# Kernel optimization log

Measured on AMD Instinct MI355X. Metric: run time of the kernel, lower is better.

Reference implementation:

```python
import jax, jax.numpy as jnp
import numpy as np

B, N, C, H, L, WSZ = 4, 16384, 1024, 16, 256, 512
Dh = C // H
Nb = N // B
NW = Nb // WSZ
EPS = 1e-6
SCALE = Dh ** -0.5


def _ln(h, g=None, b=None):
    m = h.mean(-1, keepdims=True)
    v = h.var(-1, keepdims=True)
    h = (h - m) * jax.lax.rsqrt(v + EPS)
    if g is not None:
        h = h * g + b
    return h


def setup_inputs() -> dict:
    key = jax.random.key(0)
    ks = jax.random.split(key, 16)
    s = 0.02
    return {
        'x': jax.random.normal(ks[0], (N, C), jnp.float32),
        'context': jax.random.normal(ks[1], (B, L, C), jnp.float32),
        'mod': jax.random.normal(ks[2], (B, C), jnp.float32),
        'W_mod': jax.random.normal(ks[3], (C, 6 * C), jnp.float32) * s,
        'b_mod': jnp.zeros((6 * C,), jnp.float32),
        'gamma2': jnp.ones((C,), jnp.float32),
        'beta2': jnp.zeros((C,), jnp.float32),
        'W_qkv': jax.random.normal(ks[4], (C, 3 * C), jnp.float32) * s,
        'b_qkv': jnp.zeros((3 * C,), jnp.float32),
        'W_so': jax.random.normal(ks[5], (C, C), jnp.float32) * s,
        'b_so': jnp.zeros((C,), jnp.float32),
        'W_q': jax.random.normal(ks[6], (C, C), jnp.float32) * s,
        'b_q': jnp.zeros((C,), jnp.float32),
        'W_kv': jax.random.normal(ks[7], (C, 2 * C), jnp.float32) * s,
        'b_kv': jnp.zeros((2 * C,), jnp.float32),
        'W_co': jax.random.normal(ks[8], (C, C), jnp.float32) * s,
        'b_co': jnp.zeros((C,), jnp.float32),
        'W_m1': jax.random.normal(ks[9], (C, 4 * C), jnp.float32) * s,
        'b_m1': jnp.zeros((4 * C,), jnp.float32),
        'W_m2': jax.random.normal(ks[10], (4 * C, C), jnp.float32) * s,
        'b_m2': jnp.zeros((C,), jnp.float32),
    }


def reference(x, context, mod, W_mod, b_mod, gamma2, beta2, W_qkv, b_qkv,
              W_so, b_so, W_q, b_q, W_kv, b_kv, W_co, b_co,
              W_m1, b_m1, W_m2, b_m2):
    xb = x.reshape(B, Nb, C)

    # AdaLN modulation: SiLU -> Linear -> 6 chunks, broadcast per batch item
    m6 = jax.nn.silu(mod) @ W_mod + b_mod                   # [B, 6C]
    sh_msa, sc_msa, g_msa, sh_mlp, sc_mlp, g_mlp = jnp.split(m6, 6, axis=-1)

    # --- windowed sparse self-attention ---
    h = _ln(xb) * (1.0 + sc_msa[:, None]) + sh_msa[:, None]
    qkv = (h @ W_qkv + b_qkv).reshape(B, NW, WSZ, 3, H, Dh)
    q, k, v = qkv[:, :, :, 0], qkv[:, :, :, 1], qkv[:, :, :, 2]
    a = jax.nn.softmax(jnp.einsum('bwqhd,bwkhd->bwhqk', q, k) * SCALE, axis=-1)
    o = jnp.einsum('bwhqk,bwkhd->bwqhd', a, v).reshape(B, Nb, C)
    xb = xb + g_msa[:, None] * (o @ W_so + b_so)

    # --- full cross-attention to per-batch context ---
    h = _ln(xb, gamma2, beta2)
    q = (h @ W_q + b_q).reshape(B, Nb, H, Dh)
    kv = (context @ W_kv + b_kv).reshape(B, L, 2, H, Dh)
    k, v = kv[:, :, 0], kv[:, :, 1]
    a = jax.nn.softmax(jnp.einsum('bqhd,bkhd->bhqk', q, k) * SCALE, axis=-1)
    o = jnp.einsum('bhqk,bkhd->bqhd', a, v).reshape(B, Nb, C)
    xb = xb + (o @ W_co + b_co)

    # --- modulated sparse FFN ---
    h = _ln(xb) * (1.0 + sc_mlp[:, None]) + sh_mlp[:, None]
    h = jax.nn.gelu(h @ W_m1 + b_m1, approximate=True)
    xb = xb + g_mlp[:, None] * (h @ W_m2 + b_m2)

    return xb.reshape(N, C)
```

## Files before the change

### kernel.cpp

```cpp
#include <hip/hip_runtime.h>

typedef unsigned short u16;
typedef __attribute__((ext_vector_type(8))) short short8;
typedef __attribute__((ext_vector_type(4))) float f32x4;

#define SCALE_ 0.125f

struct __align__(8) U16x4 { u16 x, y, z, w; };

__device__ __forceinline__ u16 f2b(float f) {
  union { float f; unsigned u; } c; c.f = f;
  unsigned u = c.u;
  u += 0x7fffu + ((u >> 16) & 1u);
  return (u16)(u >> 16);
}

__device__ __forceinline__ void gload16(const void* g, void* l) {
  __builtin_amdgcn_global_load_lds((const __attribute__((address_space(1))) void*)g,
                                   (__attribute__((address_space(3))) void*)l,
                                   16, 0, 0);
}

__device__ __forceinline__ float gelu_t(float x) {
  float z = 1.5957691216057308f * (x + 0.044715f * x * x * x);
  return x / (1.0f + __expf(-z));
}

__global__ __launch_bounds__(256) void wcast(const float* __restrict__ W,
                                             u16* __restrict__ Wt, int K, int N) {
  __shared__ float t[32][33];
  const int nb = N >> 5;
  const int k0 = (blockIdx.x / nb) << 5;
  const int n0 = (blockIdx.x % nb) << 5;
  const int tx = threadIdx.x & 31;
  const int ty = threadIdx.x >> 5;
#pragma unroll
  for (int r = 0; r < 32; r += 8) t[ty + r][tx] = W[(size_t)(k0 + ty + r) * N + n0 + tx];
  __syncthreads();
#pragma unroll
  for (int r = 0; r < 32; r += 8) Wt[(size_t)(n0 + ty + r) * K + k0 + tx] = f2b(t[tx][ty + r]);
}

__global__ __launch_bounds__(256) void cast_bf(const float* __restrict__ in,
                                               u16* __restrict__ out) {
  const int i = blockIdx.x * 256 + threadIdx.x;
  const float4 v = ((const float4*)in)[i];
  U16x4 o; o.x = f2b(v.x); o.y = f2b(v.y); o.z = f2b(v.z); o.w = f2b(v.w);
  ((U16x4*)out)[i] = o;
}

__global__ __launch_bounds__(256) void mod_gemm(const float* __restrict__ mod,
                                                const float* __restrict__ Wm,
                                                const float* __restrict__ bm,
                                                float* __restrict__ m6) {
  __shared__ float s[4096];
  for (int i = threadIdx.x; i < 4096; i += 256) {
    float x = mod[i];
    s[i] = x / (1.0f + __expf(-x));
  }
  __syncthreads();
  const int j = blockIdx.x * 256 + threadIdx.x;
  float a0 = bm[j], a1 = a0, a2 = a0, a3 = a0;
#pragma unroll 8
  for (int c = 0; c < 1024; c++) {
    float w = Wm[(size_t)c * 6144 + j];
    a0 += s[c] * w;
    a1 += s[1024 + c] * w;
    a2 += s[2048 + c] * w;
    a3 += s[3072 + c] * w;
  }
  m6[j] = a0; m6[6144 + j] = a1; m6[12288 + j] = a2; m6[18432 + j] = a3;
}

__global__ __launch_bounds__(256) void ln_k(const float* __restrict__ x,
                                            u16* __restrict__ out,
                                            const float* __restrict__ g,
                                            const float* __restrict__ bb,
                                            int batch_stride, int add_one) {
  const int row = blockIdx.x;
  const int tid = threadIdx.x;
  const float4 v = ((const float4*)(x + (size_t)row * 1024))[tid];
  float s = v.x + v.y + v.z + v.w;
  float q = v.x * v.x + v.y * v.y + v.z * v.z + v.w * v.w;
#pragma unroll
  for (int m = 1; m < 64; m <<= 1) {
    s += __shfl_xor(s, m, 64);
    q += __shfl_xor(q, m, 64);
  }
  __shared__ float ps[4], pq[4];
  if ((tid & 63) == 0) { ps[tid >> 6] = s; pq[tid >> 6] = q; }
  __syncthreads();
  s = ps[0] + ps[1] + ps[2] + ps[3];
  q = pq[0] + pq[1] + pq[2] + pq[3];
  const float mean = s * (1.0f / 1024.0f);
  const float var = q * (1.0f / 1024.0f) - mean * mean;
  const float rstd = rsqrtf(var + 1e-6f);
  const int batch = row >> 12;
  const float4 gv = ((const float4*)(g + (size_t)batch * batch_stride))[tid];
  const float4 bv = ((const float4*)(bb + (size_t)batch * batch_stride))[tid];
  const float ao = add_one ? 1.0f : 0.0f;
  U16x4 o;
  o.x = f2b((v.x - mean) * rstd * (gv.x + ao) + bv.x);
  o.y = f2b((v.y - mean) * rstd * (gv.y + ao) + bv.y);
  o.z = f2b((v.z - mean) * rstd * (gv.z + ao) + bv.z);
  o.w = f2b((v.w - mean) * rstd * (gv.w + ao) + bv.w);
  ((U16x4*)(out + (size_t)row * 1024))[tid] = o;
}

template <int EPI>
__global__ __launch_bounds__(256) void gemm_bt(const u16* __restrict__ A,
                                               const u16* __restrict__ Bt,
                                               const float* __restrict__ bias,
                                               void* outp, const float* res,
                                               const float* gate, int M, int N,
                                               int K, int gate_stride) {
  __shared__ __align__(16) u16 As[4096];
  __shared__ __align__(16) u16 Bs[4096];
  const int nb = N >> 7;
  const int bm = (blockIdx.x / nb) << 7;
  const int bn = (blockIdx.x % nb) << 7;
  const int tid = threadIdx.x;
  const int lane = tid & 63;
  const int wv = tid >> 6;
  const int wr = (wv >> 1) << 6;
  const int wc = (wv & 1) << 6;
  const int lrow = lane & 15;
  const int lk = lane >> 4;
  const int srow = tid >> 2;
  const int scol = (tid & 3) << 3;
  const u16* gA = A + (size_t)(bm + srow) * K + scol;
  const u16* gB = Bt + (size_t)(bn + srow) * K + scol;
  const size_t rskip = (size_t)64 * K;
  u16* lA = As + wv * 512;
  u16* lB = Bs + wv * 512;
  f32x4 acc[4][4] = {};
  for (int k0 = 0; k0 < K; k0 += 32) {
    gload16(gA + k0, lA);
    gload16(gA + k0 + rskip, lA + 2048);
    gload16(gB + k0, lB);
    gload16(gB + k0 + rskip, lB + 2048);
    __syncthreads();
    short8 a[4], b[4];
#pragma unroll
    for (int m = 0; m < 4; m++)
      a[m] = *(const short8*)(As + (wr + m * 16 + lrow) * 32 + lk * 8);
#pragma unroll
    for (int n = 0; n < 4; n++)
      b[n] = *(const short8*)(Bs + (wc + n * 16 + lrow) * 32 + lk * 8);
#pragma unroll
    for (int m = 0; m < 4; m++)
#pragma unroll
      for (int n = 0; n < 4; n++)
        acc[m][n] = __builtin_amdgcn_mfma_f32_16x16x32_bf16(a[m], b[n], acc[m][n], 0, 0, 0);
    __syncthreads();
  }
#pragma unroll
  for (int m = 0; m < 4; m++) {
    const int row0 = bm + wr + m * 16 + lk * 4;
#pragma unroll
    for (int n = 0; n < 4; n++) {
      const int col = bn + wc + n * 16 + lrow;
      const float bval = bias[col];
#pragma unroll
      for (int j = 0; j < 4; j++) {
        float v = acc[m][n][j] + bval;
        size_t idx = (size_t)(row0 + j) * N + col;
        ((u16*)outp)[idx] = f2b(v);
      }
    }
  }
}

template <int EPI>
__global__ __launch_bounds__(512, 4) void gemm2b(const u16* __restrict__ A,
                                                 const u16* __restrict__ Bt,
                                                 const float* __restrict__ bias,
                                                 void* outp, const float* res,
                                                 const float* gate, int M, int N,
                                                 int K, int gate_stride) {
  extern __shared__ char smem[];
  const int nb = N >> 8;
  const int nwg = (M >> 7) * nb;
  const int cpx = nwg >> 3;
  const int wg = (blockIdx.x & 7) * cpx + (blockIdx.x >> 3);
  const int bm = (wg / nb) << 7;
  const int bn = (wg % nb) << 8;
  const int tid = threadIdx.x;
  const int lane = tid & 63;
  const int w = tid >> 6;
  const int wm = w >> 2;
  const int wn = w & 3;
  const int lrow = lane & 15;
  const int lk = lane >> 4;
  const int u = (lane & 7) ^ (lane >> 3);
  const int r_off = w * 16 + ((lane >> 3) << 1) + (u >> 2);
  const int c_off = (u & 3) << 3;
  const u16* gA = A + (size_t)(bm + r_off) * K + c_off;
  const u16* gB = Bt + (size_t)(bn + r_off) * K + c_off;
  const size_t l_skip = (size_t)128 * K;
  char* sA = smem;
  char* sB = smem + 16384;
  const int dsb = ((lrow >> 1) << 7) + (((((lrow & 1) << 2) + lk) ^ (lrow >> 1)) << 4);
  const int aQ = wm * 4096;
  const int bQ = wn * 4096;

  f32x4 acc[4][4] = {};
  short8 af[4], bq[4];

#define SG(d, tt)                                                               \
  { gload16(gA + (size_t)(tt) * 32, sA + (d) * 8192 + w * 1024);                \
    gload16(gB + (size_t)(tt) * 32, sB + (d) * 16384 + w * 1024);               \
    gload16(gB + l_skip + (size_t)(tt) * 32, sB + (d) * 16384 + (w + 8) * 1024); }
#define RD_A(d)                                                                 \
  _Pragma("unroll") for (int m = 0; m < 4; m++)                                 \
    af[m] = *(const short8*)(sA + (d) * 8192 + aQ + m * 1024 + dsb);
#define RD_B(d)                                                                 \
  _Pragma("unroll") for (int n = 0; n < 4; n++)                                 \
    bq[n] = *(const short8*)(sB + (d) * 16384 + bQ + n * 1024 + dsb);
#define MM                                                                      \
  _Pragma("unroll") for (int m = 0; m < 4; m++)                                 \
    _Pragma("unroll") for (int n = 0; n < 4; n++)                               \
      acc[m][n] = __builtin_amdgcn_mfma_f32_16x16x32_bf16(af[m], bq[n], acc[m][n], 0, 0, 0);
#define SBAR0 __builtin_amdgcn_sched_barrier(0)
#define LGKM0 asm volatile("s_waitcnt lgkmcnt(0)" ::: "memory")
#define VM3   asm volatile("s_waitcnt vmcnt(3)" ::: "memory")

  SG(0, 0);
  const int nt = K >> 5;
  for (int t = 0; t < nt; ++t) {
    const int d = t & 1;
    const int dn = d ^ 1;
    const int tn = (t + 1 < nt) ? t + 1 : t;
    SG(dn, tn);
    SBAR0;
    VM3;
    __builtin_amdgcn_s_barrier();
    RD_A(d); RD_B(d);
    LGKM0; SBAR0;
    __builtin_amdgcn_s_setprio(1);
    MM;
    __builtin_amdgcn_s_setprio(0);
    SBAR0;
    __builtin_amdgcn_s_barrier();
  }
  asm volatile("s_waitcnt vmcnt(0)" ::: "memory");
#undef SG
#undef RD_A
#undef RD_B
#undef MM
#undef SBAR0
#undef LGKM0
#undef VM3

  const float* grow = nullptr;
  if (EPI == 2 && gate) grow = gate + (size_t)(bm >> 12) * gate_stride;
#pragma unroll
  for (int m = 0; m < 4; m++) {
    const int row0 = bm + wm * 64 + m * 16 + lk * 4;
#pragma unroll
    for (int n = 0; n < 4; n++) {
      const int col = bn + wn * 64 + n * 16 + lrow;
      const float bval = bias[col];
      float gval = 1.0f;
      if (EPI == 2 && grow) gval = grow[col];
#pragma unroll
      for (int j = 0; j < 4; j++) {
        float v = acc[m][n][j] + bval;
        size_t idx = (size_t)(row0 + j) * N + col;
        if (EPI == 0) {
          ((u16*)outp)[idx] = f2b(v);
        } else if (EPI == 1) {
          ((u16*)outp)[idx] = f2b(gelu_t(v));
        } else {
          ((float*)outp)[idx] = res[idx] + gval * v;
        }
      }
    }
  }
}

template <int MODE>
__global__ __launch_bounds__(256) void attn_k(const u16* __restrict__ QKV,
                                              const u16* __restrict__ Q2,
                                              const u16* __restrict__ KV2,
                                              u16* __restrict__ O) {
  __shared__ __align__(16) u16 Ks[4096];
  __shared__ __align__(16) u16 Vt[4096];
  __shared__ __align__(16) u16 Ps[8192];
  const int bid = blockIdx.x;
  const int tid = threadIdx.x;
  const int lane = tid & 63;
  const int wv = tid >> 6;
  const int lrow = lane & 15;
  const int lk = lane >> 4;
  const u16 *qp, *kp, *vp;
  int q_row0, q_stride, kv_row0, kv_stride, nkt, ocol;
  if (MODE == 0) {
    const int qt = bid & 3, h = (bid >> 2) & 15, w = (bid >> 6) & 7, b = bid >> 9;
    const int win = (b * 8 + w) * 512;
    q_row0 = win + qt * 128; q_stride = 3072;
    qp = QKV + h * 64;
    kp = QKV + 1024 + h * 64;
    vp = QKV + 2048 + h * 64;
    kv_row0 = win; kv_stride = 3072; nkt = 8;
    ocol = h * 64;
  } else {
    const int qt = bid & 31, h = (bid >> 5) & 15, b = bid >> 9;
    q_row0 = b * 4096 + qt * 128; q_stride = 1024;
    qp = Q2 + h * 64;
    kp = KV2 + h * 64;
    vp = KV2 + 1024 + h * 64;
    kv_row0 = b * 256; kv_stride = 2048; nkt = 4;
    ocol = h * 64;
  }
  const int qr = q_row0 + wv * 32;
  short8 qf[2][2];
#pragma unroll
  for (int m = 0; m < 2; m++)
#pragma unroll
    for (int kk = 0; kk < 2; kk++)
      qf[m][kk] = *(const short8*)(qp + (size_t)(qr + m * 16 + lrow) * q_stride + kk * 32 + lk * 8);
  f32x4 oa[2][4] = {};
  float lst[2][4];
#pragma unroll
  for (int m = 0; m < 2; m++)
#pragma unroll
    for (int j = 0; j < 4; j++) lst[m][j] = 0.0f;

  u16* Pw = Ps + wv * 2048;
  for (int kt = 0; kt < nkt; kt++) {
    const int kvr = kv_row0 + kt * 64;
    {
      const int c0 = tid;
      gload16(kp + (size_t)(kvr + (c0 >> 3)) * kv_stride + (((c0 & 7) ^ ((c0 >> 3) & 7)) << 3),
              Ks + wv * 512);
      const int c1 = tid + 256;
      gload16(kp + (size_t)(kvr + (c1 >> 3)) * kv_stride + (((c1 & 7) ^ ((c1 >> 3) & 7)) << 3),
              Ks + 2048 + wv * 512);
    }
#pragma unroll
    for (int cc = 0; cc < 2; cc++) {
      const int c = tid + cc * 256;
      const int krow = c >> 3, d0 = (c & 7) << 3;
      short8 vvv = *(const short8*)(vp + (size_t)(kvr + krow) * kv_stride + d0);
#pragma unroll
      for (int i = 0; i < 8; i++) {
        const int ii = (i + (tid & 7)) & 7;
        const int d = d0 + ii;
        Vt[d * 64 + (((krow >> 3) ^ (d & 7)) << 3) + (krow & 7)] = (u16)vvv[ii];
      }
    }
    __syncthreads();
    f32x4 s[2][4] = {};
    __builtin_amdgcn_s_setprio(1);
#pragma unroll
    for (int n = 0; n < 4; n++)
#pragma unroll
      for (int kk = 0; kk < 2; kk++) {
        short8 kb = *(const short8*)(Ks + (n * 16 + lrow) * 64 + (((kk * 4 + lk) ^ (lrow & 7)) << 3));
        s[0][n] = __builtin_amdgcn_mfma_f32_16x16x32_bf16(qf[0][kk], kb, s[0][n], 0, 0, 0);
        s[1][n] = __builtin_amdgcn_mfma_f32_16x16x32_bf16(qf[1][kk], kb, s[1][n], 0, 0, 0);
      }
    __builtin_amdgcn_s_setprio(0);
#pragma unroll
    for (int m = 0; m < 2; m++)
#pragma unroll
      for (int j = 0; j < 4; j++) {
        const float p0 = __expf(s[m][0][j] * SCALE_);
        const float p1 = __expf(s[m][1][j] * SCALE_);
        const float p2 = __expf(s[m][2][j] * SCALE_);
        const float p3 = __expf(s[m][3][j] * SCALE_);
        lst[m][j] += p0 + p1 + p2 + p3;
        const int prow = m * 16 + lk * 4 + j;
        const int base = prow * 64;
        const int r7 = prow & 7;
        const int kl = lrow >> 3, k7 = lrow & 7;
        Pw[base + (((0 + kl) ^ r7) << 3) + k7] = f2b(p0);
        Pw[base + (((2 + kl) ^ r7) << 3) + k7] = f2b(p1);
        Pw[base + (((4 + kl) ^ r7) << 3) + k7] = f2b(p2);
        Pw[base + (((6 + kl) ^ r7) << 3) + k7] = f2b(p3);
      }
#pragma unroll
    for (int kk = 0; kk < 2; kk++) {
      const int sw = ((kk * 4 + lk) ^ (lrow & 7)) << 3;
      short8 pa0 = *(const short8*)(Pw + lrow * 64 + sw);
      short8 pa1 = *(const short8*)(Pw + (16 + lrow) * 64 + sw);
      __builtin_amdgcn_s_setprio(1);
#pragma unroll
      for (int dn = 0; dn < 4; dn++) {
        short8 vb = *(const short8*)(Vt + (dn * 16 + lrow) * 64 + sw);
        oa[0][dn] = __builtin_amdgcn_mfma_f32_16x16x32_bf16(pa0, vb, oa[0][dn], 0, 0, 0);
        oa[1][dn] = __builtin_amdgcn_mfma_f32_16x16x32_bf16(pa1, vb, oa[1][dn], 0, 0, 0);
      }
      __builtin_amdgcn_s_setprio(0);
    }
    __syncthreads();
  }
#pragma unroll
  for (int m = 0; m < 2; m++)
#pragma unroll
    for (int j = 0; j < 4; j++) {
      float rs = lst[m][j];
      rs += __shfl_xor(rs, 1, 64);
      rs += __shfl_xor(rs, 2, 64);
      rs += __shfl_xor(rs, 4, 64);
      rs += __shfl_xor(rs, 8, 64);
      const float inv = 1.0f / rs;
      const int orow = qr + m * 16 + lk * 4 + j;
#pragma unroll
      for (int dn = 0; dn < 4; dn++)
        O[(size_t)orow * 1024 + ocol + dn * 16 + lrow] = f2b(oa[m][dn][j] * inv);
    }
}

extern "C" void kernel_launch(void* const* d_in, const int* in_sizes, int n_in,
                              void* d_out, int out_size, void* d_ws, size_t ws_size,
                              hipStream_t stream) {
  (void)in_sizes; (void)n_in; (void)out_size; (void)ws_size;
  const float* x      = (const float*)d_in[0];
  const float* ctx    = (const float*)d_in[1];
  const float* mod    = (const float*)d_in[2];
  const float* W_mod  = (const float*)d_in[3];
  const float* b_mod  = (const float*)d_in[4];
  const float* gamma2 = (const float*)d_in[5];
  const float* beta2  = (const float*)d_in[6];
  const float* W_qkv  = (const float*)d_in[7];
  const float* b_qkv  = (const float*)d_in[8];
  const float* W_so   = (const float*)d_in[9];
  const float* b_so   = (const float*)d_in[10];
  const float* W_q    = (const float*)d_in[11];
  const float* b_q    = (const float*)d_in[12];
  const float* W_kv   = (const float*)d_in[13];
  const float* b_kv   = (const float*)d_in[14];
  const float* W_co   = (const float*)d_in[15];
  const float* b_co   = (const float*)d_in[16];
  const float* W_m1   = (const float*)d_in[17];
  const float* b_m1   = (const float*)d_in[18];
  const float* W_m2   = (const float*)d_in[19];
  const float* b_m2   = (const float*)d_in[20];

  char* ws = (char*)d_ws;
  u16*   wt_qkv = (u16*)(ws + 0);
  u16*   wt_so  = (u16*)(ws + 6291456);
  u16*   wt_q   = (u16*)(ws + 8388608);
  u16*   wt_kv  = (u16*)(ws + 10485760);
  u16*   wt_co  = (u16*)(ws + 14680064);
  u16*   wt_m1  = (u16*)(ws + 16777216);
  u16*   wt_m2  = (u16*)(ws + 25165824);
  float* m6     = (float*)(ws + 33554432);
  u16*   ctxb   = (u16*)(ws + 33652736);
  u16*   kvb    = (u16*)(ws + 35749888);
  u16*   bufH   = (u16*)(ws + 39944192);
  u16*   bufO   = (u16*)(ws + 73498624);
  u16*   bufA   = (u16*)(ws + 107053056);
  float* xb1    = (float*)(ws + 107053056 + 50331648);
  float* outp   = (float*)d_out;

  hipFuncSetAttribute(reinterpret_cast<const void*>(&gemm2b<0>),
                      hipFuncAttributeMaxDynamicSharedMemorySize, 49152);
  hipFuncSetAttribute(reinterpret_cast<const void*>(&gemm2b<1>),
                      hipFuncAttributeMaxDynamicSharedMemorySize, 49152);
  hipFuncSetAttribute(reinterpret_cast<const void*>(&gemm2b<2>),
                      hipFuncAttributeMaxDynamicSharedMemorySize, 49152);

  wcast<<<3072, 256, 0, stream>>>(W_qkv, wt_qkv, 1024, 3072);
  wcast<<<1024, 256, 0, stream>>>(W_so,  wt_so,  1024, 1024);
  wcast<<<1024, 256, 0, stream>>>(W_q,   wt_q,   1024, 1024);
  wcast<<<2048, 256, 0, stream>>>(W_kv,  wt_kv,  1024, 2048);
  wcast<<<1024, 256, 0, stream>>>(W_co,  wt_co,  1024, 1024);
  wcast<<<4096, 256, 0, stream>>>(W_m1,  wt_m1,  1024, 4096);
  wcast<<<4096, 256, 0, stream>>>(W_m2,  wt_m2,  4096, 1024);
  cast_bf<<<1024, 256, 0, stream>>>(ctx, ctxb);

  mod_gemm<<<24, 256, 0, stream>>>(mod, W_mod, b_mod, m6);

  ln_k<<<16384, 256, 0, stream>>>(x, bufH, m6 + 1024, m6 + 0, 6144, 1);
  gemm2b<0><<<1536, 512, 49152, stream>>>(bufH, wt_qkv, b_qkv, bufA, nullptr, nullptr, 16384, 3072, 1024, 0);
  attn_k<0><<<2048, 256, 0, stream>>>(bufA, nullptr, nullptr, bufO);
  gemm2b<2><<<512, 512, 49152, stream>>>(bufO, wt_so, b_so, xb1, x, m6 + 2048, 16384, 1024, 1024, 6144);

  ln_k<<<16384, 256, 0, stream>>>(xb1, bufH, gamma2, beta2, 0, 0);
  gemm2b<0><<<512, 512, 49152, stream>>>(bufH, wt_q, b_q, bufA, nullptr, nullptr, 16384, 1024, 1024, 0);
  gemm_bt<0><<<128, 256, 0, stream>>>(ctxb, wt_kv, b_kv, kvb, nullptr, nullptr, 1024, 2048, 1024, 0);
  attn_k<1><<<2048, 256, 0, stream>>>(nullptr, bufA, kvb, bufO);
  gemm2b<2><<<512, 512, 49152, stream>>>(bufO, wt_co, b_co, outp, xb1, nullptr, 16384, 1024, 1024, 0);

  ln_k<<<16384, 256, 0, stream>>>(outp, bufH, m6 + 4096, m6 + 3072, 6144, 1);
  gemm2b<1><<<2048, 512, 49152, stream>>>(bufH, wt_m1, b_m1, bufA, nullptr, nullptr, 16384, 4096, 1024, 0);
  gemm2b<2><<<512, 512, 49152, stream>>>(bufA, wt_m2, b_m2, outp, outp, m6 + 5120, 16384, 1024, 4096, 6144);
}
```

Before: 1.001 ms.

## Triple-buffer GEMM LDS pipeline and double attention block size to 512 threads

The GEMM main loop moves from a two-stage to a three-stage LDS ring buffer. It prefetches two K-tiles ahead and waits with vmcnt(6) instead of vmcnt(3), so more global-load latency can hide behind MFMA work. Dynamic LDS per block grows from 48KB to 72KB to hold the extra stage, which may limit how many blocks fit per CU. Separately, the attention kernels now use 512-thread blocks that each cover 256 query rows with half as many blocks, so each loaded K/V tile serves twice as many queries.

```diff
diff --git a/kernel.cpp b/kernel.cpp
--- a/kernel.cpp
+++ b/kernel.cpp
@@ -199,7 +199,7 @@
   const u16* gB = Bt + (size_t)(bn + r_off) * K + c_off;
   const size_t l_skip = (size_t)128 * K;
   char* sA = smem;
-  char* sB = smem + 16384;
+  char* sB = smem + 24576;
   const int dsb = ((lrow >> 1) << 7) + (((((lrow & 1) << 2) + lk) ^ (lrow >> 1)) << 4);
   const int aQ = wm * 4096;
   const int bQ = wn * 4096;
@@ -223,17 +223,18 @@
       acc[m][n] = __builtin_amdgcn_mfma_f32_16x16x32_bf16(af[m], bq[n], acc[m][n], 0, 0, 0);
 #define SBAR0 __builtin_amdgcn_sched_barrier(0)
 #define LGKM0 asm volatile("s_waitcnt lgkmcnt(0)" ::: "memory")
-#define VM3   asm volatile("s_waitcnt vmcnt(3)" ::: "memory")
-
+#define VM6   asm volatile("s_waitcnt vmcnt(6)" ::: "memory")
+
+  const int nt = K >> 5;
   SG(0, 0);
-  const int nt = K >> 5;
+  SG(1, (1 < nt) ? 1 : 0);
+  int d = 0;
   for (int t = 0; t < nt; ++t) {
-    const int d = t & 1;
-    const int dn = d ^ 1;
-    const int tn = (t + 1 < nt) ? t + 1 : t;
-    SG(dn, tn);
+    const int d2 = (d + 2 >= 3) ? d - 1 : d + 2;
+    const int tn = (t + 2 < nt) ? t + 2 : nt - 1;
+    SG(d2, tn);
     SBAR0;
-    VM3;
+    VM6;
     __builtin_amdgcn_s_barrier();
     RD_A(d); RD_B(d);
     LGKM0; SBAR0;
@@ -242,6 +243,7 @@
     __builtin_amdgcn_s_setprio(0);
     SBAR0;
     __builtin_amdgcn_s_barrier();
+    d = (d + 1 >= 3) ? 0 : d + 1;
   }
   asm volatile("s_waitcnt vmcnt(0)" ::: "memory");
 #undef SG
@@ -250,7 +252,7 @@
 #undef MM
 #undef SBAR0
 #undef LGKM0
-#undef VM3
+#undef VM6
 
   const float* grow = nullptr;
   if (EPI == 2 && gate) grow = gate + (size_t)(bm >> 12) * gate_stride;
@@ -280,13 +282,13 @@
 }
 
 template <int MODE>
-__global__ __launch_bounds__(256) void attn_k(const u16* __restrict__ QKV,
+__global__ __launch_bounds__(512) void attn_k(const u16* __restrict__ QKV,
                                               const u16* __restrict__ Q2,
                                               const u16* __restrict__ KV2,
                                               u16* __restrict__ O) {
   __shared__ __align__(16) u16 Ks[4096];
   __shared__ __align__(16) u16 Vt[4096];
-  __shared__ __align__(16) u16 Ps[8192];
+  __shared__ __align__(16) u16 Ps[16384];
   const int bid = blockIdx.x;
   const int tid = threadIdx.x;
   const int lane = tid & 63;
@@ -296,17 +298,17 @@
   const u16 *qp, *kp, *vp;
   int q_row0, q_stride, kv_row0, kv_stride, nkt, ocol;
   if (MODE == 0) {
-    const int qt = bid & 3, h = (bid >> 2) & 15, w = (bid >> 6) & 7, b = bid >> 9;
+    const int qt = bid & 1, h = (bid >> 1) & 15, w = (bid >> 5) & 7, b = bid >> 8;
     const int win = (b * 8 + w) * 512;
-    q_row0 = win + qt * 128; q_stride = 3072;
+    q_row0 = win + qt * 256; q_stride = 3072;
     qp = QKV + h * 64;
     kp = QKV + 1024 + h * 64;
     vp = QKV + 2048 + h * 64;
     kv_row0 = win; kv_stride = 3072; nkt = 8;
     ocol = h * 64;
   } else {
-    const int qt = bid & 31, h = (bid >> 5) & 15, b = bid >> 9;
-    q_row0 = b * 4096 + qt * 128; q_stride = 1024;
+    const int qt = bid & 15, h = (bid >> 4) & 15, b = bid >> 8;
+    q_row0 = b * 4096 + qt * 256; q_stride = 1024;
     qp = Q2 + h * 64;
     kp = KV2 + h * 64;
     vp = KV2 + 1024 + h * 64;
@@ -331,23 +333,18 @@
   for (int kt = 0; kt < nkt; kt++) {
     const int kvr = kv_row0 + kt * 64;
     {
-      const int c0 = tid;
-      gload16(kp + (size_t)(kvr + (c0 >> 3)) * kv_stride + (((c0 & 7) ^ ((c0 >> 3) & 7)) << 3),
+      const int r = tid >> 3, c = tid & 7;
+      gload16(kp + (size_t)(kvr + r) * kv_stride + (((c) ^ (r & 7)) << 3),
               Ks + wv * 512);
-      const int c1 = tid + 256;
-      gload16(kp + (size_t)(kvr + (c1 >> 3)) * kv_stride + (((c1 & 7) ^ ((c1 >> 3) & 7)) << 3),
-              Ks + 2048 + wv * 512);
-    }
-#pragma unroll
-    for (int cc = 0; cc < 2; cc++) {
-      const int c = tid + cc * 256;
-      const int krow = c >> 3, d0 = (c & 7) << 3;
+    }
+    {
+      const int krow = tid >> 3, d0 = (tid & 7) << 3;
       short8 vvv = *(const short8*)(vp + (size_t)(kvr + krow) * kv_stride + d0);
 #pragma unroll
       for (int i = 0; i < 8; i++) {
         const int ii = (i + (tid & 7)) & 7;
-        const int d = d0 + ii;
-        Vt[d * 64 + (((krow >> 3) ^ (d & 7)) << 3) + (krow & 7)] = (u16)vvv[ii];
+        const int dd = d0 + ii;
+        Vt[dd * 64 + (((krow >> 3) ^ (dd & 7)) << 3) + (krow & 7)] = (u16)vvv[ii];
       }
     }
     __syncthreads();
@@ -457,11 +454,11 @@
   float* outp   = (float*)d_out;
 
   hipFuncSetAttribute(reinterpret_cast<const void*>(&gemm2b<0>),
-                      hipFuncAttributeMaxDynamicSharedMemorySize, 49152);
+                      hipFuncAttributeMaxDynamicSharedMemorySize, 73728);
   hipFuncSetAttribute(reinterpret_cast<const void*>(&gemm2b<1>),
-                      hipFuncAttributeMaxDynamicSharedMemorySize, 49152);
+                      hipFuncAttributeMaxDynamicSharedMemorySize, 73728);
   hipFuncSetAttribute(reinterpret_cast<const void*>(&gemm2b<2>),
-                      hipFuncAttributeMaxDynamicSharedMemorySize, 49152);
+                      hipFuncAttributeMaxDynamicSharedMemorySize, 73728);
 
   wcast<<<3072, 256, 0, stream>>>(W_qkv, wt_qkv, 1024, 3072);
   wcast<<<1024, 256, 0, stream>>>(W_so,  wt_so,  1024, 1024);
@@ -475,17 +472,17 @@
   mod_gemm<<<24, 256, 0, stream>>>(mod, W_mod, b_mod, m6);
 
   ln_k<<<16384, 256, 0, stream>>>(x, bufH, m6 + 1024, m6 + 0, 6144, 1);
-  gemm2b<0><<<1536, 512, 49152, stream>>>(bufH, wt_qkv, b_qkv, bufA, nullptr, nullptr, 16384, 3072, 1024, 0);
-  attn_k<0><<<2048, 256, 0, stream>>>(bufA, nullptr, nullptr, bufO);
-  gemm2b<2><<<512, 512, 49152, stream>>>(bufO, wt_so, b_so, xb1, x, m6 + 2048, 16384, 1024, 1024, 6144);
+  gemm2b<0><<<1536, 512, 73728, stream>>>(bufH, wt_qkv, b_qkv, bufA, nullptr, nullptr, 16384, 3072, 1024, 0);
+  attn_k<0><<<1024, 512, 0, stream>>>(bufA, nullptr, nullptr, bufO);
+  gemm2b<2><<<512, 512, 73728, stream>>>(bufO, wt_so, b_so, xb1, x, m6 + 2048, 16384, 1024, 1024, 6144);
 
   ln_k<<<16384, 256, 0, stream>>>(xb1, bufH, gamma2, beta2, 0, 0);
-  gemm2b<0><<<512, 512, 49152, stream>>>(bufH, wt_q, b_q, bufA, nullptr, nullptr, 16384, 1024, 1024, 0);
+  gemm2b<0><<<512, 512, 73728, stream>>>(bufH, wt_q, b_q, bufA, nullptr, nullptr, 16384, 1024, 1024, 0);
   gemm_bt<0><<<128, 256, 0, stream>>>(ctxb, wt_kv, b_kv, kvb, nullptr, nullptr, 1024, 2048, 1024, 0);
-  attn_k<1><<<2048, 256, 0, stream>>>(nullptr, bufA, kvb, bufO);
-  gemm2b<2><<<512, 512, 49152, stream>>>(bufO, wt_co, b_co, outp, xb1, nullptr, 16384, 1024, 1024, 0);
+  attn_k<1><<<1024, 512, 0, stream>>>(nullptr, bufA, kvb, bufO);
+  gemm2b<2><<<512, 512, 73728, stream>>>(bufO, wt_co, b_co, outp, xb1, nullptr, 16384, 1024, 1024, 0);
 
   ln_k<<<16384, 256, 0, stream>>>(outp, bufH, m6 + 4096, m6 + 3072, 6144, 1);
-  gemm2b<1><<<2048, 512, 49152, stream>>>(bufH, wt_m1, b_m1, bufA, nullptr, nullptr, 16384, 4096, 1024, 0);
-  gemm2b<2><<<512, 512, 49152, stream>>>(bufA, wt_m2, b_m2, outp, outp, m6 + 5120, 16384, 1024, 4096, 6144);
-}
+  gemm2b<1><<<2048, 512, 73728, stream>>>(bufH, wt_m1, b_m1, bufA, nullptr, nullptr, 16384, 4096, 1024, 0);
+  gemm2b<2><<<512, 512, 73728, stream>>>(bufA, wt_m2, b_m2, outp, outp, m6 + 5120, 16384, 1024, 4096, 6144);
+}
```

New measurement: 1.003 ms. Within noise of the previous version (+0.2%).
